# Kernel optimization log

Measured on AMD Instinct MI355X. Metric: run time of the kernel, lower is better.

Reference implementation:

```python
import jax, jax.numpy as jnp
import numpy as np

B, H, S, D = 2, 12, 2048, 64


def setup_inputs() -> dict:
    key = jax.random.key(0)
    kq, kk, kv = jax.random.split(key, 3)
    q = jax.random.normal(kq, (B, H, S, D), dtype=jnp.float32)
    k = jax.random.normal(kk, (B, H, S, D), dtype=jnp.float32)
    v = jax.random.normal(kv, (B, H, S, D), dtype=jnp.float32)
    # causal mask: True = attend (keep), lower triangle
    mask = jnp.tril(jnp.ones((S, S), dtype=bool))
    return {"q": q, "k": k, "v": v, "mask": mask}


def reference(q, k, v, mask):
    dim = q.shape[-1]
    # [B,H,S,S] scores
    scores = jnp.einsum("bhqd,bhkd->bhqk", q, k) / jnp.sqrt(jnp.asarray(dim, q.dtype))
    # dynamic mask-direction logic from the original module:
    # if the mask is denser in the strict upper triangle, True means "mask out";
    # otherwise True means "keep".
    sq = mask.shape[-1]
    sample = mask.reshape(-1, sq, sq)[0]
    upper = jnp.triu(jnp.ones_like(sample, dtype=bool), k=1)
    flip = jnp.sum(sample & upper) > jnp.sum(sample & ~upper)
    keep = jnp.where(flip, ~mask, mask)  # True = keep
    neg_inf = jnp.asarray(-jnp.inf, scores.dtype)
    scores = jnp.where(keep, scores, neg_inf)
    weights = jax.nn.softmax(scores, axis=-1)
    # dropout with p_drop=0.0 is the identity
    return jnp.einsum("bhqk,bhkd->bhqd", weights, v)
```

## Files before the change

### kernel.cpp

```cpp
#include <hip/hip_runtime.h>
#include <hip/hip_bf16.h>


#define SEQ 2048
#define DH 64
#define NHEADS 24
#define BN 64
#define LDK 72
#define ELEMS_PER_TENSOR (NHEADS * SEQ * DH)
#define NSLOT10 (NHEADS * 16 * 8)
#define WS_KV    ((size_t)2 * ELEMS_PER_TENSOR * 2)
#define WS_FA10  (WS_KV + (size_t)NSLOT10 * 8192 * 2 + (size_t)NSLOT10 * 128 * 4)

typedef float f32x4 __attribute__((ext_vector_type(4)));
typedef __bf16 bf16x8 __attribute__((ext_vector_type(8)));
typedef __bf16 bf16x4 __attribute__((ext_vector_type(4)));

#if __has_builtin(__builtin_amdgcn_exp2f)
#define EXP2F(x) __builtin_amdgcn_exp2f(x)
#else
#define EXP2F(x) exp2f(x)
#endif

#define QSCALE 0.1803368801111204f

__global__ __launch_bounds__(256)
void prep_kernel(const float* __restrict__ k, const float* __restrict__ v,
                 __bf16* __restrict__ ks, __bf16* __restrict__ vt)
{
    __shared__ __bf16 T[64][LDK];
    const int bx = blockIdx.x;
    const int tid = threadIdx.x;
    if (bx < 1536) {
        const int idx = (bx * 256 + tid) * 8;
        f32x4 a = *(const f32x4*)(k + idx);
        f32x4 b = *(const f32x4*)(k + idx + 4);
        bf16x8 o;
        #pragma unroll
        for (int j = 0; j < 4; ++j) { o[j] = (__bf16)a[j]; o[4 + j] = (__bf16)b[j]; }
        *(bf16x8*)(ks + idx) = o;
    } else {
        const int b2 = bx - 1536;
        const int bh = b2 >> 5;
        const int s0 = (b2 & 31) * 64;
        const int r = tid >> 2, c0 = (tid & 3) * 16;
        const float* vp = v + (size_t)bh * SEQ * DH + (size_t)(s0 + r) * DH + c0;
        __bf16 tmp[16];
        #pragma unroll
        for (int jj = 0; jj < 16; ++jj) tmp[jj] = (__bf16)vp[jj];
        *(bf16x8*)&T[r][c0]     = *(bf16x8*)&tmp[0];
        *(bf16x8*)&T[r][c0 + 8] = *(bf16x8*)&tmp[8];
        __syncthreads();
        const int d = tid >> 2, j0 = (tid & 3) * 16;
        __bf16 o[16];
        #pragma unroll
        for (int jj = 0; jj < 16; ++jj) o[jj] = T[j0 + jj][d];
        __bf16* op = vt + (size_t)bh * DH * SEQ + (size_t)d * SEQ + s0 + j0;
        *(bf16x8*)op       = *(bf16x8*)&o[0];
        *(bf16x8*)(op + 8) = *(bf16x8*)&o[8];
    }
}

__global__ __launch_bounds__(256, 3)
void fa10_kernel(const float* __restrict__ q, const __bf16* __restrict__ ks,
                 const __bf16* __restrict__ vt,
                 __bf16* __restrict__ opart, float* __restrict__ lpart)
{
    const int bx = blockIdx.x;
    const int xcd = bx & 7;
    const int sub = bx >> 3;
    const int bh = (sub / 72) * 8 + xcd;
    const int i = sub % 72;
    int mt2, ch;
    if      (i < 8)  { mt2 = 15; ch = i; }
    else if (i < 16) { mt2 = 14; ch = i - 8; }
    else if (i < 23) { mt2 = 13; ch = i - 16; }
    else if (i < 30) { mt2 = 12; ch = i - 23; }
    else if (i < 36) { mt2 = 11; ch = i - 30; }
    else if (i < 42) { mt2 = 10; ch = i - 36; }
    else if (i < 47) { mt2 = 9;  ch = i - 42; }
    else if (i < 52) { mt2 = 8;  ch = i - 47; }
    else if (i < 56) { mt2 = 7;  ch = i - 52; }
    else if (i < 60) { mt2 = 6;  ch = i - 56; }
    else if (i < 63) { mt2 = 5;  ch = i - 60; }
    else if (i < 66) { mt2 = 4;  ch = i - 63; }
    else if (i < 68) { mt2 = 3;  ch = i - 66; }
    else if (i < 70) { mt2 = 2;  ch = i - 68; }
    else if (i < 71) { mt2 = 1;  ch = 0; }
    else             { mt2 = 0;  ch = 0; }
    const int jt0 = ch * 4;
    const int jt_end = min(jt0 + 4, 2 * mt2 + 2);
    const int q0 = mt2 * 128;

    const int tid = threadIdx.x;
    const int w = tid >> 6, lane = tid & 63;
    const int g = lane >> 4, li = lane & 15;

    __shared__ __bf16 Ks[2][64 * 64];
    __shared__ __bf16 Vs[2][64 * 64];
    __shared__ __bf16 Ps[4 * 32 * 64];

    const __bf16* kh = ks + (size_t)bh * SEQ * DH;
    const __bf16* vh = vt + (size_t)bh * DH * SEQ;

    bf16x8 qf[2][2];
    #pragma unroll
    for (int a = 0; a < 2; ++a) {
        const float* qp = q + (size_t)bh * SEQ * DH +
                          (size_t)(q0 + w * 32 + a * 16 + li) * DH + g * 8;
        #pragma unroll
        for (int c = 0; c < 2; ++c) {
            f32x4 x0 = *(const f32x4*)(qp + c * 32);
            f32x4 x1 = *(const f32x4*)(qp + c * 32 + 4);
            #pragma unroll
            for (int j = 0; j < 4; ++j) {
                qf[a][c][j]     = (__bf16)(x0[j] * QSCALE);
                qf[a][c][4 + j] = (__bf16)(x1[j] * QSCALE);
            }
        }
    }

    bf16x8 ones;
    #pragma unroll
    for (int j = 0; j < 8; ++j) ones[j] = (__bf16)1.0f;

    f32x4 acc[2][4] = {};
    f32x4 accl[2] = {};

    const int srow0 = tid >> 3;
    const int sg    = tid & 7;

    bf16x8 kr[2], vr[2];
    #pragma unroll
    for (int s = 0; s < 2; ++s) {
        const int row = s * 32 + srow0;
        const int lg = sg ^ (row & 7);
        kr[s] = *(const bf16x8*)(kh + (size_t)(jt0 * BN + row) * DH + lg * 8);
        vr[s] = *(const bf16x8*)(vh + (size_t)row * SEQ + jt0 * BN + lg * 8);
    }
    #pragma unroll
    for (int s = 0; s < 2; ++s) {
        *(bf16x8*)((char*)Ks[0] + s * 4096 + tid * 16) = kr[s];
        *(bf16x8*)((char*)Vs[0] + s * 4096 + tid * 16) = vr[s];
    }
    if (jt0 + 1 < jt_end) {
        const int kv1 = (jt0 + 1) * BN;
        #pragma unroll
        for (int s = 0; s < 2; ++s) {
            const int row = s * 32 + srow0;
            const int lg = sg ^ (row & 7);
            kr[s] = *(const bf16x8*)(kh + (size_t)(kv1 + row) * DH + lg * 8);
            vr[s] = *(const bf16x8*)(vh + (size_t)row * SEQ + kv1 + lg * 8);
        }
    }
    __syncthreads();

    int buf = 0;
    for (int jt = jt0; jt < jt_end; ++jt) {
        if (jt + 1 < jt_end) {
            #pragma unroll
            for (int s = 0; s < 2; ++s) {
                *(bf16x8*)((char*)Ks[buf ^ 1] + s * 4096 + tid * 16) = kr[s];
                *(bf16x8*)((char*)Vs[buf ^ 1] + s * 4096 + tid * 16) = vr[s];
            }
        }
        if (jt + 2 < jt_end) {
            const int kv2 = (jt + 2) * BN;
            #pragma unroll
            for (int s = 0; s < 2; ++s) {
                const int row = s * 32 + srow0;
                const int lg = sg ^ (row & 7);
                kr[s] = *(const bf16x8*)(kh + (size_t)(kv2 + row) * DH + lg * 8);
                vr[s] = *(const bf16x8*)(vh + (size_t)row * SEQ + kv2 + lg * 8);
            }
        }

        const char* Kb = (const char*)Ks[buf];
        const char* Vb = (const char*)Vs[buf];
        float s4[2][4][4];
        #pragma unroll
        for (int t = 0; t < 4; ++t) {
            f32x4 sa0 = {}, sa1 = {};
            #pragma unroll
            for (int c = 0; c < 2; ++c) {
                bf16x8 kf = *(const bf16x8*)(Kb +
                    (t * 16 + li) * 128 + (((c * 4 + g) ^ (li & 7)) << 4));
                sa0 = __builtin_amdgcn_mfma_f32_16x16x32_bf16(kf, qf[0][c], sa0, 0, 0, 0);
                sa1 = __builtin_amdgcn_mfma_f32_16x16x32_bf16(kf, qf[1][c], sa1, 0, 0, 0);
            }
            #pragma unroll
            for (int r = 0; r < 4; ++r) { s4[0][t][r] = sa0[r]; s4[1][t][r] = sa1[r]; }
        }

        if (jt >= 2 * mt2) {
            #pragma unroll
            for (int a = 0; a < 2; ++a) {
                const int qr = q0 + w * 32 + a * 16 + li;
                #pragma unroll
                for (int t = 0; t < 4; ++t) {
                    #pragma unroll
                    for (int r = 0; r < 4; ++r)
                        if (jt * 64 + t * 16 + g * 4 + r > qr) s4[a][t][r] = -1e30f;
                }
            }
        }

        #pragma unroll
        for (int a = 0; a < 2; ++a) {
            const int row = a * 16 + li;
            #pragma unroll
            for (int t = 0; t < 4; ++t) {
                bf16x4 p4;
                #pragma unroll
                for (int r = 0; r < 4; ++r) p4[r] = (__bf16)EXP2F(s4[a][t][r]);
                const int pg = (t * 2 + (g >> 1)) ^ (li & 7);
                *(bf16x4*)((char*)Ps + w * 4096 + row * 128 + (pg << 4) + ((g & 1) << 3)) = p4;
            }
        }

        #pragma unroll
        for (int c = 0; c < 2; ++c) {
            const int pgp = ((c * 4 + g) ^ (li & 7)) << 4;
            bf16x8 pf0 = *(const bf16x8*)((const char*)Ps + w * 4096 + li * 128 + pgp);
            bf16x8 pf1 = *(const bf16x8*)((const char*)Ps + w * 4096 + (16 + li) * 128 + pgp);
            accl[0] = __builtin_amdgcn_mfma_f32_16x16x32_bf16(pf0, ones, accl[0], 0, 0, 0);
            accl[1] = __builtin_amdgcn_mfma_f32_16x16x32_bf16(pf1, ones, accl[1], 0, 0, 0);
            #pragma unroll
            for (int t = 0; t < 4; ++t) {
                bf16x8 vf = *(const bf16x8*)(Vb + (t * 16 + li) * 128 + pgp);
                acc[0][t] = __builtin_amdgcn_mfma_f32_16x16x32_bf16(pf0, vf, acc[0][t], 0, 0, 0);
                acc[1][t] = __builtin_amdgcn_mfma_f32_16x16x32_bf16(pf1, vf, acc[1][t], 0, 0, 0);
            }
        }

        if (jt + 1 < jt_end) __syncthreads();
        buf ^= 1;
    }

    const int slot = (bh * 16 + mt2) * 8 + ch;
    __bf16* po = opart + (size_t)slot * 8192;
    #pragma unroll
    for (int a = 0; a < 2; ++a) {
        #pragma unroll
        for (int r = 0; r < 4; ++r) {
            const int row = w * 32 + a * 16 + g * 4 + r;
            __bf16* op = po + row * 64 + li;
            #pragma unroll
            for (int t = 0; t < 4; ++t) op[t * 16] = (__bf16)acc[a][t][r];
            if (li == 0) lpart[(size_t)slot * 128 + row] = accl[a][r];
        }
    }
}

__global__ __launch_bounds__(256)
void fa_reduce(const __bf16* __restrict__ opart, const float* __restrict__ lpart,
               float* __restrict__ out)
{
    const int bx = blockIdx.x;
    const int bh = bx >> 4, mt2 = bx & 15;
    const int nc = (mt2 + 2) >> 1;
    const int base = (bh * 16 + mt2) * 8;
    const int tid = threadIdx.x;
    #pragma unroll
    for (int rnd = 0; rnd < 8; ++rnd) {
        const int flat = rnd * 1024 + tid * 4;
        const int row = flat >> 6;
        float o0 = 0, o1 = 0, o2 = 0, o3 = 0, l = 0;
        for (int c = 0; c < nc; ++c) {
            bf16x4 ov = *(const bf16x4*)(opart + (size_t)(base + c) * 8192 + flat);
            o0 += (float)ov[0]; o1 += (float)ov[1]; o2 += (float)ov[2]; o3 += (float)ov[3];
            l += lpart[(size_t)(base + c) * 128 + row];
        }
        const float inv = 1.0f / l;
        f32x4 res = { o0 * inv, o1 * inv, o2 * inv, o3 * inv };
        *(f32x4*)(out + (size_t)bh * SEQ * DH + (size_t)mt2 * 8192 + flat) = res;
    }
}

__global__ __launch_bounds__(256, 2)
void fa_causal_kernel(const float* __restrict__ q, const float* __restrict__ k,
                      const float* __restrict__ v, float* __restrict__ out)
{
    const int mt = 31 - (blockIdx.x & 31);
    const int bh = blockIdx.x >> 5;
    const int tid = threadIdx.x;
    const int w = tid >> 6, lane = tid & 63;
    const int g = lane >> 4, li = lane & 15;
    const int m0 = mt * 64;
    __shared__ __bf16 KsF[BN][LDK];
    __shared__ __bf16 VsF[DH][LDK];
    __shared__ __bf16 PsF[4][16][LDK];
    const size_t head_off = (size_t)bh * SEQ * DH;
    const float* qh = q + head_off;
    const float* kh = k + head_off;
    const float* vh = v + head_off;
    float* oh = out + head_off;
    const int qrow = m0 + w * 16 + li;
    bf16x8 qf[2];
    {
        const float* qp = qh + (size_t)qrow * DH + g * 8;
        #pragma unroll
        for (int c = 0; c < 2; ++c) {
            const float* p = qp + c * 32;
            #pragma unroll
            for (int jj = 0; jj < 8; ++jj) qf[c][jj] = (__bf16)p[jj];
        }
    }
    f32x4 acc[4] = {};
    float mrow[4], lrow[4];
    #pragma unroll
    for (int r = 0; r < 4; ++r) { mrow[r] = -1e30f; lrow[r] = 0.0f; }
    const float scale = 0.125f;
    const int srow = tid >> 2, scol = (tid & 3) * 16;
    for (int jt = 0; jt <= mt; ++jt) {
        const int kv0 = jt * BN;
        __syncthreads();
        {
            const float* kp = kh + (size_t)(kv0 + srow) * DH + scol;
            __bf16 tmp[16];
            #pragma unroll
            for (int jj = 0; jj < 16; ++jj) tmp[jj] = (__bf16)kp[jj];
            *(bf16x8*)&KsF[srow][scol]     = *(bf16x8*)&tmp[0];
            *(bf16x8*)&KsF[srow][scol + 8] = *(bf16x8*)&tmp[8];
            const float* vp = vh + (size_t)(kv0 + srow) * DH + scol;
            #pragma unroll
            for (int jj = 0; jj < 16; ++jj) VsF[scol + jj][srow] = (__bf16)vp[jj];
        }
        __syncthreads();
        float s4[4][4];
        #pragma unroll
        for (int t = 0; t < 4; ++t) {
            f32x4 sa = {};
            #pragma unroll
            for (int c = 0; c < 2; ++c) {
                bf16x8 kfr = *(const bf16x8*)&KsF[t * 16 + li][c * 32 + g * 8];
                sa = __builtin_amdgcn_mfma_f32_16x16x32_bf16(qf[c], kfr, sa, 0, 0, 0);
            }
            #pragma unroll
            for (int r = 0; r < 4; ++r) s4[t][r] = sa[r] * scale;
        }
        if (jt == mt) {
            #pragma unroll
            for (int t = 0; t < 4; ++t) {
                const int col = kv0 + t * 16 + li;
                #pragma unroll
                for (int r = 0; r < 4; ++r)
                    if (col > m0 + w * 16 + g * 4 + r) s4[t][r] = -1e30f;
            }
        }
        #pragma unroll
        for (int r = 0; r < 4; ++r) {
            float mx = fmaxf(fmaxf(s4[0][r], s4[1][r]), fmaxf(s4[2][r], s4[3][r]));
            #pragma unroll
            for (int off = 1; off < 16; off <<= 1)
                mx = fmaxf(mx, __shfl_xor(mx, off, 64));
            const float mnew = fmaxf(mrow[r], mx);
            const float alpha = __expf(mrow[r] - mnew);
            mrow[r] = mnew;
            float ps = 0.0f;
            #pragma unroll
            for (int t = 0; t < 4; ++t) {
                const float p = __expf(s4[t][r] - mnew);
                s4[t][r] = p;
                ps += p;
            }
            #pragma unroll
            for (int off = 1; off < 16; off <<= 1)
                ps += __shfl_xor(ps, off, 64);
            lrow[r] = lrow[r] * alpha + ps;
            #pragma unroll
            for (int t = 0; t < 4; ++t) acc[t][r] *= alpha;
        }
        #pragma unroll
        for (int t = 0; t < 4; ++t)
            #pragma unroll
            for (int r = 0; r < 4; ++r)
                PsF[w][g * 4 + r][t * 16 + li] = (__bf16)s4[t][r];
        __syncthreads();
        #pragma unroll
        for (int c = 0; c < 2; ++c) {
            bf16x8 pf = *(const bf16x8*)&PsF[w][li][c * 32 + g * 8];
            #pragma unroll
            for (int t = 0; t < 4; ++t) {
                bf16x8 vfr = *(const bf16x8*)&VsF[t * 16 + li][c * 32 + g * 8];
                acc[t] = __builtin_amdgcn_mfma_f32_16x16x32_bf16(pf, vfr, acc[t], 0, 0, 0);
            }
        }
    }
    #pragma unroll
    for (int r = 0; r < 4; ++r) {
        const int row = m0 + w * 16 + g * 4 + r;
        const float inv = 1.0f / lrow[r];
        float* op = oh + (size_t)row * DH + li;
        #pragma unroll
        for (int t = 0; t < 4; ++t) op[t * 16] = acc[t][r] * inv;
    }
}

extern "C" void kernel_launch(void* const* d_in, const int* in_sizes, int n_in,
                              void* d_out, int out_size, void* d_ws, size_t ws_size,
                              hipStream_t stream) {
    (void)in_sizes; (void)n_in; (void)out_size;
    const float* q = (const float*)d_in[0];
    const float* k = (const float*)d_in[1];
    const float* v = (const float*)d_in[2];
    float* out = (float*)d_out;

    if (ws_size >= WS_FA10) {
        __bf16* ks = (__bf16*)d_ws;
        __bf16* vt = ks + ELEMS_PER_TENSOR;
        __bf16* opart = (__bf16*)((char*)d_ws + WS_KV);
        float* lpart = (float*)((char*)d_ws + WS_KV + (size_t)NSLOT10 * 8192 * 2);
        prep_kernel<<<dim3(1536 + 768), dim3(256), 0, stream>>>(k, v, ks, vt);
        fa10_kernel<<<dim3(1728), dim3(256), 0, stream>>>(q, ks, vt, opart, lpart);
        fa_reduce<<<dim3(NHEADS * 16), dim3(256), 0, stream>>>(opart, lpart, out);
    } else {
        fa_causal_kernel<<<dim3(NHEADS * 32), dim3(256), 0, stream>>>(q, k, v, out);
    }
}
```

Before: 139.0 us.

## Use 8-tile KV chunks, write short rows directly, reduce only split rows

Each split-K work item now covers 8 KV tiles instead of 4, which cuts the grid from 1728 to 960 blocks and reduces partial-result traffic. Query tiles with at most 8 KV tiles (mt2<4) skip the partial buffers and write normalized fp32 output directly. The reduce kernel launches only for the remaining tiles, using an XCD-aware index. The trade is less parallelism and coarser load balance per block, in exchange for fewer partial writes and reads and a smaller reduce.

```diff
diff --git a/kernel.cpp b/kernel.cpp
--- a/kernel.cpp
+++ b/kernel.cpp
@@ -8,9 +8,9 @@
 #define BN 64
 #define LDK 72
 #define ELEMS_PER_TENSOR (NHEADS * SEQ * DH)
-#define NSLOT10 (NHEADS * 16 * 8)
+#define NSLOT (NHEADS * 16 * 4)
 #define WS_KV    ((size_t)2 * ELEMS_PER_TENSOR * 2)
-#define WS_FA10  (WS_KV + (size_t)NSLOT10 * 8192 * 2 + (size_t)NSLOT10 * 128 * 4)
+#define WS_FA11  (WS_KV + (size_t)NSLOT * 8192 * 2 + (size_t)NSLOT * 128 * 4)
 
 typedef float f32x4 __attribute__((ext_vector_type(4)));
 typedef __bf16 bf16x8 __attribute__((ext_vector_type(8)));
@@ -62,34 +62,33 @@
 }
 
 __global__ __launch_bounds__(256, 3)
-void fa10_kernel(const float* __restrict__ q, const __bf16* __restrict__ ks,
+void fa11_kernel(const float* __restrict__ q, const __bf16* __restrict__ ks,
                  const __bf16* __restrict__ vt,
-                 __bf16* __restrict__ opart, float* __restrict__ lpart)
+                 __bf16* __restrict__ opart, float* __restrict__ lpart,
+                 float* __restrict__ out)
 {
     const int bx = blockIdx.x;
     const int xcd = bx & 7;
     const int sub = bx >> 3;
-    const int bh = (sub / 72) * 8 + xcd;
-    const int i = sub % 72;
-    int mt2, ch;
-    if      (i < 8)  { mt2 = 15; ch = i; }
-    else if (i < 16) { mt2 = 14; ch = i - 8; }
-    else if (i < 23) { mt2 = 13; ch = i - 16; }
-    else if (i < 30) { mt2 = 12; ch = i - 23; }
-    else if (i < 36) { mt2 = 11; ch = i - 30; }
-    else if (i < 42) { mt2 = 10; ch = i - 36; }
-    else if (i < 47) { mt2 = 9;  ch = i - 42; }
-    else if (i < 52) { mt2 = 8;  ch = i - 47; }
-    else if (i < 56) { mt2 = 7;  ch = i - 52; }
-    else if (i < 60) { mt2 = 6;  ch = i - 56; }
-    else if (i < 63) { mt2 = 5;  ch = i - 60; }
-    else if (i < 66) { mt2 = 4;  ch = i - 63; }
-    else if (i < 68) { mt2 = 3;  ch = i - 66; }
-    else if (i < 70) { mt2 = 2;  ch = i - 68; }
-    else if (i < 71) { mt2 = 1;  ch = 0; }
-    else             { mt2 = 0;  ch = 0; }
-    const int jt0 = ch * 4;
-    const int jt_end = min(jt0 + 4, 2 * mt2 + 2);
+    const int bh = (sub / 40) * 8 + xcd;
+    const int rem = 39 - (sub % 40);
+    int mt2, st;
+    if      (rem >= 36) { mt2 = 15; st = 36; }
+    else if (rem >= 32) { mt2 = 14; st = 32; }
+    else if (rem >= 28) { mt2 = 13; st = 28; }
+    else if (rem >= 24) { mt2 = 12; st = 24; }
+    else if (rem >= 21) { mt2 = 11; st = 21; }
+    else if (rem >= 18) { mt2 = 10; st = 18; }
+    else if (rem >= 15) { mt2 = 9;  st = 15; }
+    else if (rem >= 12) { mt2 = 8;  st = 12; }
+    else if (rem >= 10) { mt2 = 7;  st = 10; }
+    else if (rem >= 8)  { mt2 = 6;  st = 8; }
+    else if (rem >= 6)  { mt2 = 5;  st = 6; }
+    else if (rem >= 4)  { mt2 = 4;  st = 4; }
+    else                { mt2 = rem; st = rem; }
+    const int chunk = rem - st;
+    const int jt0 = chunk * 8;
+    const int jt_end = min(jt0 + 8, 2 * mt2 + 2);
     const int q0 = mt2 * 128;
 
     const int tid = threadIdx.x;
@@ -237,17 +236,32 @@
         buf ^= 1;
     }
 
-    const int slot = (bh * 16 + mt2) * 8 + ch;
-    __bf16* po = opart + (size_t)slot * 8192;
-    #pragma unroll
-    for (int a = 0; a < 2; ++a) {
-        #pragma unroll
-        for (int r = 0; r < 4; ++r) {
-            const int row = w * 32 + a * 16 + g * 4 + r;
-            __bf16* op = po + row * 64 + li;
-            #pragma unroll
-            for (int t = 0; t < 4; ++t) op[t * 16] = (__bf16)acc[a][t][r];
-            if (li == 0) lpart[(size_t)slot * 128 + row] = accl[a][r];
+    if (2 * mt2 + 2 <= 8) {
+        float* oh = out + (size_t)bh * SEQ * DH;
+        #pragma unroll
+        for (int a = 0; a < 2; ++a) {
+            #pragma unroll
+            for (int r = 0; r < 4; ++r) {
+                const int row = q0 + w * 32 + a * 16 + g * 4 + r;
+                const float inv = 1.0f / accl[a][r];
+                float* op = oh + (size_t)row * DH + li;
+                #pragma unroll
+                for (int t = 0; t < 4; ++t) op[t * 16] = acc[a][t][r] * inv;
+            }
+        }
+    } else {
+        const int slot = (bh * 16 + mt2) * 4 + chunk;
+        __bf16* po = opart + (size_t)slot * 8192;
+        #pragma unroll
+        for (int a = 0; a < 2; ++a) {
+            #pragma unroll
+            for (int r = 0; r < 4; ++r) {
+                const int row = w * 32 + a * 16 + g * 4 + r;
+                __bf16* op = po + row * 64 + li;
+                #pragma unroll
+                for (int t = 0; t < 4; ++t) op[t * 16] = (__bf16)acc[a][t][r];
+                if (li == 0) lpart[(size_t)slot * 128 + row] = accl[a][r];
+            }
         }
     }
 }
@@ -257,9 +271,12 @@
                float* __restrict__ out)
 {
     const int bx = blockIdx.x;
-    const int bh = bx >> 4, mt2 = bx & 15;
-    const int nc = (mt2 + 2) >> 1;
-    const int base = (bh * 16 + mt2) * 8;
+    const int xcd = bx & 7;
+    const int r2 = bx >> 3;
+    const int bh = (r2 / 12) * 8 + xcd;
+    const int mt2 = 4 + (r2 % 12);
+    const int nc = (mt2 >> 2) + 1;
+    const int base = (bh * 16 + mt2) * 4;
     const int tid = threadIdx.x;
     #pragma unroll
     for (int rnd = 0; rnd < 8; ++rnd) {
@@ -406,14 +423,14 @@
     const float* v = (const float*)d_in[2];
     float* out = (float*)d_out;
 
-    if (ws_size >= WS_FA10) {
+    if (ws_size >= WS_FA11) {
         __bf16* ks = (__bf16*)d_ws;
         __bf16* vt = ks + ELEMS_PER_TENSOR;
         __bf16* opart = (__bf16*)((char*)d_ws + WS_KV);
-        float* lpart = (float*)((char*)d_ws + WS_KV + (size_t)NSLOT10 * 8192 * 2);
+        float* lpart = (float*)((char*)d_ws + WS_KV + (size_t)NSLOT * 8192 * 2);
         prep_kernel<<<dim3(1536 + 768), dim3(256), 0, stream>>>(k, v, ks, vt);
-        fa10_kernel<<<dim3(1728), dim3(256), 0, stream>>>(q, ks, vt, opart, lpart);
-        fa_reduce<<<dim3(NHEADS * 16), dim3(256), 0, stream>>>(opart, lpart, out);
+        fa11_kernel<<<dim3(960), dim3(256), 0, stream>>>(q, ks, vt, opart, lpart, out);
+        fa_reduce<<<dim3(288), dim3(256), 0, stream>>>(opart, lpart, out);
     } else {
         fa_causal_kernel<<<dim3(NHEADS * 32), dim3(256), 0, stream>>>(q, k, v, out);
     }
```

After: 131.1 us. 5.7% less time.
